# Performance work log

Hardware: AMD Instinct MI355X
Metric: run time of the kernel (lower is better)

The kernel has to match this reference:

```python
import jax, jax.numpy as jnp
import numpy as np

N = 100000   # nodes
E = 1600000  # edges (avg degree 16)
D = 32       # feature dim

def setup_inputs() -> dict:
    key = jax.random.key(0)
    k1, k2, k3, k4 = jax.random.split(key, 4)
    feat = jax.random.normal(k1, (N, D), dtype=jnp.float32)
    e_feat = jax.random.normal(k2, (E, 1), dtype=jnp.float32)
    src = jax.random.randint(k3, (E,), 0, N)
    dst = jax.random.randint(k4, (E,), 0, N)
    return {"feat": feat, "e_feat": e_feat, "src": src, "dst": dst}

def reference(feat, e_feat, src, dst):
    n = feat.shape[0]
    ones = jnp.ones(src.shape[0], dtype=feat.dtype)
    # degrees computed on the full graph (before self-loop removal), as in DGL code
    out_deg = jax.ops.segment_sum(ones, src, num_segments=n)
    in_deg = jax.ops.segment_sum(ones, dst, num_segments=n)
    src_norm = jnp.power(jnp.clip(out_deg, 1.0, None), -0.5)[:, None]  # [N,1]
    dst_norm = jnp.power(jnp.clip(in_deg, 1.0, None), -0.5)[:, None]   # [N,1]
    # remove_self_loop: mask out self-loop edges in the aggregation only
    mask = (src != dst).astype(feat.dtype)[:, None]                    # [E,1]
    # u_mul_e: gather normalized src features, multiply by edge weight
    msg = (feat * src_norm)[src] * (e_feat * mask)                     # [E,D]
    agg = jax.ops.segment_sum(msg, dst, num_segments=n)                # [N,D]
    out = feat - agg * dst_norm
    return jnp.sum(jnp.abs(out), axis=1)                               # [N]
```

## Files before the change

### kernel.cpp

```cpp
#include <hip/hip_runtime.h>

#define D 32
#define RANGE 128
#define RMAX 800
#define JC 512
#define CHUNKMAX 3200
#define CAP 2304
#define SJC 128
#define SCHUNKMAX 12800

__global__ __launch_bounds__(512) void sort_src(
        const int* __restrict__ src,
        unsigned* __restrict__ srcs, unsigned* __restrict__ metaS,
        int E, int R, int chunkS) {
    __shared__ unsigned ids[SCHUNKMAX];
    __shared__ int cs[RMAX];
    __shared__ int cur[RMAX];
    int j = blockIdx.x, t = threadIdx.x;
    int e0 = j * chunkS, e1 = min(E, e0 + chunkS), cntE = e1 - e0;
    for (int i = t; i < RMAX; i += 512) cs[i] = 0;
    __syncthreads();
    for (int e = e0 + 2 * t; e < e1; e += 1024) {
        if (e + 1 < e1) {
            int2 s2 = *(const int2*)(src + e);
            atomicAdd(&cs[s2.x >> 7], 1);
            atomicAdd(&cs[s2.y >> 7], 1);
        } else {
            atomicAdd(&cs[src[e] >> 7], 1);
        }
    }
    __syncthreads();
    {
        int i1 = t + 512;
        cur[t] = cs[t];
        if (i1 < RMAX) cur[i1] = cs[i1];
        __syncthreads();
        for (int off = 1; off < RMAX; off <<= 1) {
            int v0 = (t >= off) ? cur[t - off] : 0;
            int v1 = 0;
            if (i1 < RMAX && i1 >= off) v1 = cur[i1 - off];
            __syncthreads();
            cur[t] += v0;
            if (i1 < RMAX) cur[i1] += v1;
            __syncthreads();
        }
        cur[t] -= cs[t];
        if (i1 < RMAX) cur[i1] -= cs[i1];
        __syncthreads();
    }
    for (int e = e0 + t; e < e1; e += 512) {
        unsigned s = (unsigned)src[e];
        int pos = atomicAdd(&cur[s >> 7], 1);
        ids[pos] = s;
    }
    __syncthreads();
    size_t baseE = (size_t)j * chunkS;
    for (int i = t; i < cntE; i += 512) srcs[baseE + i] = ids[i];
    for (int i = t; i < R; i += 512)
        metaS[(size_t)j * R + i] =
            ((unsigned)(cur[i] - cs[i]) << 16) | (unsigned)cs[i];
}

__global__ __launch_bounds__(512) void sort_chunks(
        const int* __restrict__ src, const int* __restrict__ dst,
        const float* __restrict__ ef,
        uint2* __restrict__ recs, unsigned* __restrict__ metaD,
        int E, int R, int chunk) {
    __shared__ uint2 sd[CHUNKMAX];
    __shared__ int cd[RMAX];
    __shared__ int curD[RMAX];
    int j = blockIdx.x, t = threadIdx.x;
    int e0 = j * chunk, e1 = min(E, e0 + chunk), cntE = e1 - e0;
    for (int i = t; i < RMAX; i += 512) cd[i] = 0;
    __syncthreads();
    for (int e = e0 + 2 * t; e < e1; e += 1024) {
        if (e + 1 < e1) {
            int2 d2 = *(const int2*)(dst + e);
            atomicAdd(&cd[d2.x >> 7], 1);
            atomicAdd(&cd[d2.y >> 7], 1);
        } else {
            atomicAdd(&cd[dst[e] >> 7], 1);
        }
    }
    __syncthreads();
    {
        int i1 = t + 512;
        curD[t] = cd[t];
        if (i1 < RMAX) curD[i1] = cd[i1];
        __syncthreads();
        for (int off = 1; off < RMAX; off <<= 1) {
            int v0 = (t >= off) ? curD[t - off] : 0;
            int v1 = 0;
            if (i1 < RMAX && i1 >= off) v1 = curD[i1 - off];
            __syncthreads();
            curD[t] += v0;
            if (i1 < RMAX) curD[i1] += v1;
            __syncthreads();
        }
        curD[t] -= cd[t];
        if (i1 < RMAX) curD[i1] -= cd[i1];
        __syncthreads();
    }
    for (int e = e0 + t; e < e1; e += 512) {
        int s = src[e], d = dst[e];
        float w = (s == d) ? 0.0f : ef[e];
        int pos = atomicAdd(&curD[d >> 7], 1);
        sd[pos] = make_uint2((unsigned)s | ((unsigned)(d & (RANGE - 1)) << 17),
                             __float_as_uint(w));
    }
    __syncthreads();
    size_t baseE = (size_t)j * chunk;
    for (int i = t; i < cntE; i += 512) recs[baseE + i] = sd[i];
    for (int i = t; i < R; i += 512)
        metaD[(size_t)i * JC + j] =
            ((unsigned)(curD[i] - cd[i]) << 16) | (unsigned)cd[i];
}

__device__ __forceinline__ unsigned short f2bf(float x) {
    unsigned u = __float_as_uint(x);
    u += 0x7FFFu + ((u >> 16) & 1u);
    return (unsigned short)(u >> 16);
}

__global__ __launch_bounds__(512) void srcnorm_convert(
        const unsigned* __restrict__ srcs, const unsigned* __restrict__ metaS,
        const float* __restrict__ feat, unsigned short* __restrict__ featb,
        int n, int R, int chunkS) {
    __shared__ int cnt[RANGE];
    __shared__ unsigned meta[SJC];
    int r = blockIdx.x, t = threadIdx.x;
    int base = r * RANGE, lim = min(n - base, RANGE);
    if (t < RANGE) cnt[t] = 0;
    if (t < SJC) meta[t] = metaS[(size_t)t * R + r];
    __syncthreads();
    int seg = t >> 2, sub = t & 3;
    {
        unsigned m = meta[seg];
        int st = m >> 16, c = m & 0xFFFFu;
        const unsigned* p = srcs + (size_t)seg * chunkS + st;
        for (int k = sub; k < c; k += 4)
            atomicAdd(&cnt[p[k] - (unsigned)base], 1);
    }
    __syncthreads();
    int total4 = lim * 8;
    for (int i = t; i < total4; i += 512) {
        int row = i >> 3;
        float sn = rsqrtf((float)max(cnt[row], 1));
        float4 f = ((const float4*)(feat + (size_t)(base + row) * D))[i & 7];
        ushort4 u;
        u.x = f2bf(f.x * sn); u.y = f2bf(f.y * sn);
        u.z = f2bf(f.z * sn); u.w = f2bf(f.w * sn);
        ((ushort4*)(featb + (size_t)(base + row) * D))[i & 7] = u;
    }
}

__global__ __launch_bounds__(512) void gather_kernel(
        const float* __restrict__ feat, const unsigned short* __restrict__ featb,
        const uint2* __restrict__ recs, const unsigned* __restrict__ metaD,
        float* __restrict__ out, int n, int R, int chunk) {
    __shared__ uint2 raw[CAP];
    __shared__ uint2 srec[CAP];
    __shared__ int segpre[JC + 1];
    __shared__ int indeg[RANGE];
    __shared__ int pre[RANGE + 1];
    int r = blockIdx.x, t = threadIdx.x;
    int base = r * RANGE, lim = min(n - base, RANGE);
    unsigned m = metaD[(size_t)r * JC + t];
    int st = m >> 16, c = m & 0xFFFFu;
    segpre[t + 1] = c;
    if (t == 0) segpre[0] = 0;
    if (t < RANGE) indeg[t] = 0;
    __syncthreads();
    for (int off = 1; off < JC; off <<= 1) {
        int v = (t + 1 > off) ? segpre[t + 1 - off] : 0;
        __syncthreads();
        segpre[t + 1] += v;
        __syncthreads();
    }
    int total = segpre[JC];
    bool ovf = total > CAP;
    const uint2* p = recs + (size_t)t * chunk + st;
    if (!ovf) {
        int dp = segpre[t];
        for (int k = 0; k < c; k++) {
            uint2 rec = p[k];
            raw[dp + k] = rec;
            atomicAdd(&indeg[rec.x >> 17], 1);
        }
    } else {
        for (int k = 0; k < c; k++) atomicAdd(&indeg[p[k].x >> 17], 1);
    }
    __syncthreads();
    if (t < RANGE) pre[t + 1] = indeg[t];
    if (t == 0) pre[0] = 0;
    __syncthreads();
    for (int off = 1; off < RANGE; off <<= 1) {
        int v = 0;
        if (t < RANGE) { int idx = t + 1; if (idx > off) v = pre[idx - off]; }
        __syncthreads();
        if (t < RANGE) pre[t + 1] += v;
        __syncthreads();
    }
    if (t < RANGE) indeg[t] = pre[t];
    __syncthreads();
    if (!ovf) {
        for (int i = t; i < total; i += 512) {
            uint2 rec = raw[i];
            int dl = rec.x >> 17;
            int pos = atomicAdd(&indeg[dl], 1);
            srec[pos] = make_uint2(rec.x & 0x1FFFFu, rec.y);
        }
    }
    __syncthreads();
    int node = t >> 2;
    int cch = t & 3;
    if (node >= lim) return;
    int p0i = pre[node];
    int cnt = pre[node + 1] - p0i;
    float a0 = 0.f, a1 = 0.f, a2 = 0.f, a3 = 0.f, a4 = 0.f, a5 = 0.f, a6 = 0.f, a7 = 0.f;
    if (!ovf) {
        const uint2* sp = srec + p0i;
        int i = 0;
        for (; i + 4 <= cnt; i += 4) {
            uint2 q0 = sp[i], q1 = sp[i + 1], q2 = sp[i + 2], q3 = sp[i + 3];
            uint4 b0 = ((const uint4*)(featb + (size_t)q0.x * D))[cch];
            uint4 b1 = ((const uint4*)(featb + (size_t)q1.x * D))[cch];
            uint4 b2 = ((const uint4*)(featb + (size_t)q2.x * D))[cch];
            uint4 b3 = ((const uint4*)(featb + (size_t)q3.x * D))[cch];
            float w0 = __uint_as_float(q0.y), w1 = __uint_as_float(q1.y);
            float w2 = __uint_as_float(q2.y), w3 = __uint_as_float(q3.y);
            a0 += __uint_as_float(b0.x << 16) * w0 + __uint_as_float(b1.x << 16) * w1
                + __uint_as_float(b2.x << 16) * w2 + __uint_as_float(b3.x << 16) * w3;
            a1 += __uint_as_float(b0.x & 0xFFFF0000u) * w0 + __uint_as_float(b1.x & 0xFFFF0000u) * w1
                + __uint_as_float(b2.x & 0xFFFF0000u) * w2 + __uint_as_float(b3.x & 0xFFFF0000u) * w3;
            a2 += __uint_as_float(b0.y << 16) * w0 + __uint_as_float(b1.y << 16) * w1
                + __uint_as_float(b2.y << 16) * w2 + __uint_as_float(b3.y << 16) * w3;
            a3 += __uint_as_float(b0.y & 0xFFFF0000u) * w0 + __uint_as_float(b1.y & 0xFFFF0000u) * w1
                + __uint_as_float(b2.y & 0xFFFF0000u) * w2 + __uint_as_float(b3.y & 0xFFFF0000u) * w3;
            a4 += __uint_as_float(b0.z << 16) * w0 + __uint_as_float(b1.z << 16) * w1
                + __uint_as_float(b2.z << 16) * w2 + __uint_as_float(b3.z << 16) * w3;
            a5 += __uint_as_float(b0.z & 0xFFFF0000u) * w0 + __uint_as_float(b1.z & 0xFFFF0000u) * w1
                + __uint_as_float(b2.z & 0xFFFF0000u) * w2 + __uint_as_float(b3.z & 0xFFFF0000u) * w3;
            a6 += __uint_as_float(b0.w << 16) * w0 + __uint_as_float(b1.w << 16) * w1
                + __uint_as_float(b2.w << 16) * w2 + __uint_as_float(b3.w << 16) * w3;
            a7 += __uint_as_float(b0.w & 0xFFFF0000u) * w0 + __uint_as_float(b1.w & 0xFFFF0000u) * w1
                + __uint_as_float(b2.w & 0xFFFF0000u) * w2 + __uint_as_float(b3.w & 0xFFFF0000u) * w3;
        }
        for (; i < cnt; i++) {
            uint2 q = sp[i];
            uint4 b = ((const uint4*)(featb + (size_t)q.x * D))[cch];
            float w = __uint_as_float(q.y);
            a0 += __uint_as_float(b.x << 16) * w;
            a1 += __uint_as_float(b.x & 0xFFFF0000u) * w;
            a2 += __uint_as_float(b.y << 16) * w;
            a3 += __uint_as_float(b.y & 0xFFFF0000u) * w;
            a4 += __uint_as_float(b.z << 16) * w;
            a5 += __uint_as_float(b.z & 0xFFFF0000u) * w;
            a6 += __uint_as_float(b.w << 16) * w;
            a7 += __uint_as_float(b.w & 0xFFFF0000u) * w;
        }
    } else {
        for (int j = 0; j < JC; j++) {
            unsigned mm = metaD[(size_t)r * JC + j];
            const uint2* pp = recs + (size_t)j * chunk + (mm >> 16);
            int cc = mm & 0xFFFFu;
            for (int k = 0; k < cc; k++) {
                uint2 rec = pp[k];
                if ((int)(rec.x >> 17) == node) {
                    uint4 b = ((const uint4*)(featb + (size_t)(rec.x & 0x1FFFFu) * D))[cch];
                    float w = __uint_as_float(rec.y);
                    a0 += __uint_as_float(b.x << 16) * w;
                    a1 += __uint_as_float(b.x & 0xFFFF0000u) * w;
                    a2 += __uint_as_float(b.y << 16) * w;
                    a3 += __uint_as_float(b.y & 0xFFFF0000u) * w;
                    a4 += __uint_as_float(b.z << 16) * w;
                    a5 += __uint_as_float(b.z & 0xFFFF0000u) * w;
                    a6 += __uint_as_float(b.w << 16) * w;
                    a7 += __uint_as_float(b.w & 0xFFFF0000u) * w;
                }
            }
        }
    }
    float dn = rsqrtf((float)max(cnt, 1));
    const float4* fr = (const float4*)(feat + (size_t)(base + node) * D);
    float4 fA = fr[cch * 2];
    float4 fB = fr[cch * 2 + 1];
    float v = fabsf(fA.x - a0 * dn) + fabsf(fA.y - a1 * dn) +
              fabsf(fA.z - a2 * dn) + fabsf(fA.w - a3 * dn) +
              fabsf(fB.x - a4 * dn) + fabsf(fB.y - a5 * dn) +
              fabsf(fB.z - a6 * dn) + fabsf(fB.w - a7 * dn);
    v += __shfl_xor(v, 1, 4);
    v += __shfl_xor(v, 2, 4);
    if (cch == 0) out[base + node] = v;
}

extern "C" void kernel_launch(void* const* d_in, const int* in_sizes, int n_in,
                              void* d_out, int out_size, void* d_ws, size_t ws_size,
                              hipStream_t stream) {
    const float* feat   = (const float*)d_in[0];
    const float* e_feat = (const float*)d_in[1];
    const int*   src    = (const int*)d_in[2];
    const int*   dst    = (const int*)d_in[3];
    const int E = in_sizes[2];
    const int n = in_sizes[0] / D;
    float* out = (float*)d_out;

    const int R = (n + RANGE - 1) / RANGE;
    const int chunk  = (((E + JC  - 1) / JC ) + 1) & ~1;
    const int chunkS = (((E + SJC - 1) / SJC) + 1) & ~1;

    char* p = (char*)d_ws;
    uint2* recs     = (uint2*)p;    p += ((size_t)JC * chunk * 8 + 15) & ~(size_t)15;
    unsigned* metaD = (unsigned*)p; p += ((size_t)R * JC * 4 + 15) & ~(size_t)15;
    unsigned* srcs  = (unsigned*)p; p += ((size_t)SJC * chunkS * 4 + 15) & ~(size_t)15;
    unsigned* metaS = (unsigned*)p; p += ((size_t)SJC * R * 4 + 15) & ~(size_t)15;
    unsigned short* featb = (unsigned short*)p;

    sort_src<<<SJC, 512, 0, stream>>>(src, srcs, metaS, E, R, chunkS);

    sort_chunks<<<JC, 512, 0, stream>>>(src, dst, e_feat, recs, metaD, E, R, chunk);

    srcnorm_convert<<<R, 512, 0, stream>>>(srcs, metaS, feat, featb, n, R, chunkS);

    gather_kernel<<<R, 512, 0, stream>>>(feat, featb, recs, metaD, out, n, R, chunk);
}
```

Measured before the change: 145.5 us.

## Fuse src and dst bucket sorts into one launch and use wave-shuffle scans

The two bucketing kernels (source-degree sort and destination-record sort) become a single launch in which block index picks the role, so both run concurrently and one launch is saved. The source sort is split into twice as many smaller chunks (SJC 256) to fit a shared arena and balance work. All shared-memory Hillis-Steele prefix scans are replaced by a 64-lane shuffle-based scan with a per-wave partial array, which cuts barrier counts. The trade-off is that the src blocks now share occupancy with the dst blocks, and srcnorm reads more, smaller segments.

Result: faster. 139.3 us (-4.3%).

```diff
diff --git a/kernel.cpp b/kernel.cpp
--- a/kernel.cpp
+++ b/kernel.cpp
@@ -6,114 +6,113 @@
 #define JC 512
 #define CHUNKMAX 3200
 #define CAP 2304
-#define SJC 128
-#define SCHUNKMAX 12800
-
-__global__ __launch_bounds__(512) void sort_src(
-        const int* __restrict__ src,
-        unsigned* __restrict__ srcs, unsigned* __restrict__ metaS,
-        int E, int R, int chunkS) {
-    __shared__ unsigned ids[SCHUNKMAX];
-    __shared__ int cs[RMAX];
-    __shared__ int cur[RMAX];
-    int j = blockIdx.x, t = threadIdx.x;
-    int e0 = j * chunkS, e1 = min(E, e0 + chunkS), cntE = e1 - e0;
-    for (int i = t; i < RMAX; i += 512) cs[i] = 0;
-    __syncthreads();
-    for (int e = e0 + 2 * t; e < e1; e += 1024) {
-        if (e + 1 < e1) {
-            int2 s2 = *(const int2*)(src + e);
-            atomicAdd(&cs[s2.x >> 7], 1);
-            atomicAdd(&cs[s2.y >> 7], 1);
-        } else {
-            atomicAdd(&cs[src[e] >> 7], 1);
-        }
-    }
-    __syncthreads();
-    {
-        int i1 = t + 512;
-        cur[t] = cs[t];
-        if (i1 < RMAX) cur[i1] = cs[i1];
-        __syncthreads();
-        for (int off = 1; off < RMAX; off <<= 1) {
-            int v0 = (t >= off) ? cur[t - off] : 0;
-            int v1 = 0;
-            if (i1 < RMAX && i1 >= off) v1 = cur[i1 - off];
-            __syncthreads();
-            cur[t] += v0;
-            if (i1 < RMAX) cur[i1] += v1;
-            __syncthreads();
-        }
-        cur[t] -= cs[t];
-        if (i1 < RMAX) cur[i1] -= cs[i1];
-        __syncthreads();
-    }
-    for (int e = e0 + t; e < e1; e += 512) {
-        unsigned s = (unsigned)src[e];
-        int pos = atomicAdd(&cur[s >> 7], 1);
-        ids[pos] = s;
-    }
-    __syncthreads();
-    size_t baseE = (size_t)j * chunkS;
-    for (int i = t; i < cntE; i += 512) srcs[baseE + i] = ids[i];
-    for (int i = t; i < R; i += 512)
-        metaS[(size_t)j * R + i] =
-            ((unsigned)(cur[i] - cs[i]) << 16) | (unsigned)cs[i];
-}
-
-__global__ __launch_bounds__(512) void sort_chunks(
+#define SJC 256
+#define SCHUNKMAX 6400
+
+__device__ __forceinline__ int scan512(int x, int* wp, int t) {
+    int lane = t & 63, w = t >> 6;
+    #pragma unroll
+    for (int d = 1; d < 64; d <<= 1) {
+        int y = __shfl_up(x, d, 64);
+        if (lane >= d) x += y;
+    }
+    if (lane == 63) wp[w] = x;
+    __syncthreads();
+    int off = 0;
+    #pragma unroll
+    for (int i = 0; i < 7; i++) if (i < w) off += wp[i];
+    return x + off;
+}
+
+__global__ __launch_bounds__(512) void fused_sort(
         const int* __restrict__ src, const int* __restrict__ dst,
         const float* __restrict__ ef,
         uint2* __restrict__ recs, unsigned* __restrict__ metaD,
-        int E, int R, int chunk) {
-    __shared__ uint2 sd[CHUNKMAX];
-    __shared__ int cd[RMAX];
-    __shared__ int curD[RMAX];
-    int j = blockIdx.x, t = threadIdx.x;
-    int e0 = j * chunk, e1 = min(E, e0 + chunk), cntE = e1 - e0;
-    for (int i = t; i < RMAX; i += 512) cd[i] = 0;
-    __syncthreads();
-    for (int e = e0 + 2 * t; e < e1; e += 1024) {
-        if (e + 1 < e1) {
-            int2 d2 = *(const int2*)(dst + e);
-            atomicAdd(&cd[d2.x >> 7], 1);
-            atomicAdd(&cd[d2.y >> 7], 1);
-        } else {
-            atomicAdd(&cd[dst[e] >> 7], 1);
-        }
-    }
-    __syncthreads();
-    {
+        unsigned* __restrict__ srcs, unsigned* __restrict__ metaS,
+        int E, int R, int chunk, int chunkS) {
+    __shared__ __align__(16) char arena[32000];
+    __shared__ int wp[8];
+    int t = threadIdx.x;
+    int* cnt = (int*)(arena + 25600);
+    int* cur = (int*)(arena + 28800);
+
+    if (blockIdx.x < JC) {
+        int j = blockIdx.x;
+        uint2* sd = (uint2*)arena;
+        int e0 = j * chunk, e1 = min(E, e0 + chunk), cntE = e1 - e0;
+        for (int i = t; i < RMAX; i += 512) cnt[i] = 0;
+        __syncthreads();
+        for (int e = e0 + 2 * t; e < e1; e += 1024) {
+            if (e + 1 < e1) {
+                int2 d2 = *(const int2*)(dst + e);
+                atomicAdd(&cnt[d2.x >> 7], 1);
+                atomicAdd(&cnt[d2.y >> 7], 1);
+            } else {
+                atomicAdd(&cnt[dst[e] >> 7], 1);
+            }
+        }
+        __syncthreads();
+        int v0 = cnt[t];
+        int incl0 = scan512(v0, wp, t);
+        int tot0 = wp[0] + wp[1] + wp[2] + wp[3] + wp[4] + wp[5] + wp[6] + wp[7];
+        __syncthreads();
         int i1 = t + 512;
-        curD[t] = cd[t];
-        if (i1 < RMAX) curD[i1] = cd[i1];
-        __syncthreads();
-        for (int off = 1; off < RMAX; off <<= 1) {
-            int v0 = (t >= off) ? curD[t - off] : 0;
-            int v1 = 0;
-            if (i1 < RMAX && i1 >= off) v1 = curD[i1 - off];
-            __syncthreads();
-            curD[t] += v0;
-            if (i1 < RMAX) curD[i1] += v1;
-            __syncthreads();
-        }
-        curD[t] -= cd[t];
-        if (i1 < RMAX) curD[i1] -= cd[i1];
-        __syncthreads();
-    }
-    for (int e = e0 + t; e < e1; e += 512) {
-        int s = src[e], d = dst[e];
-        float w = (s == d) ? 0.0f : ef[e];
-        int pos = atomicAdd(&curD[d >> 7], 1);
-        sd[pos] = make_uint2((unsigned)s | ((unsigned)(d & (RANGE - 1)) << 17),
-                             __float_as_uint(w));
-    }
-    __syncthreads();
-    size_t baseE = (size_t)j * chunk;
-    for (int i = t; i < cntE; i += 512) recs[baseE + i] = sd[i];
-    for (int i = t; i < R; i += 512)
-        metaD[(size_t)i * JC + j] =
-            ((unsigned)(curD[i] - cd[i]) << 16) | (unsigned)cd[i];
+        int v1 = (i1 < RMAX) ? cnt[i1] : 0;
+        int incl1 = scan512(v1, wp, t);
+        cur[t] = incl0 - v0;
+        if (i1 < RMAX) cur[i1] = tot0 + incl1 - v1;
+        __syncthreads();
+        for (int e = e0 + t; e < e1; e += 512) {
+            int s = src[e], d = dst[e];
+            float w = (s == d) ? 0.0f : ef[e];
+            int pos = atomicAdd(&cur[d >> 7], 1);
+            sd[pos] = make_uint2((unsigned)s | ((unsigned)(d & (RANGE - 1)) << 17),
+                                 __float_as_uint(w));
+        }
+        __syncthreads();
+        size_t baseE = (size_t)j * chunk;
+        for (int i = t; i < cntE; i += 512) recs[baseE + i] = sd[i];
+        for (int i = t; i < R; i += 512)
+            metaD[(size_t)i * JC + j] =
+                ((unsigned)(cur[i] - cnt[i]) << 16) | (unsigned)cnt[i];
+    } else {
+        int j = blockIdx.x - JC;
+        unsigned* ids = (unsigned*)arena;
+        int e0 = j * chunkS, e1 = min(E, e0 + chunkS), cntE = e1 - e0;
+        for (int i = t; i < RMAX; i += 512) cnt[i] = 0;
+        __syncthreads();
+        for (int e = e0 + 2 * t; e < e1; e += 1024) {
+            if (e + 1 < e1) {
+                int2 s2 = *(const int2*)(src + e);
+                atomicAdd(&cnt[s2.x >> 7], 1);
+                atomicAdd(&cnt[s2.y >> 7], 1);
+            } else {
+                atomicAdd(&cnt[src[e] >> 7], 1);
+            }
+        }
+        __syncthreads();
+        int v0 = cnt[t];
+        int incl0 = scan512(v0, wp, t);
+        int tot0 = wp[0] + wp[1] + wp[2] + wp[3] + wp[4] + wp[5] + wp[6] + wp[7];
+        __syncthreads();
+        int i1 = t + 512;
+        int v1 = (i1 < RMAX) ? cnt[i1] : 0;
+        int incl1 = scan512(v1, wp, t);
+        cur[t] = incl0 - v0;
+        if (i1 < RMAX) cur[i1] = tot0 + incl1 - v1;
+        __syncthreads();
+        for (int e = e0 + t; e < e1; e += 512) {
+            unsigned s = (unsigned)src[e];
+            int pos = atomicAdd(&cur[s >> 7], 1);
+            ids[pos] = s;
+        }
+        __syncthreads();
+        size_t baseE = (size_t)j * chunkS;
+        for (int i = t; i < cntE; i += 512) srcs[baseE + i] = ids[i];
+        for (int i = t; i < R; i += 512)
+            metaS[(size_t)j * R + i] =
+                ((unsigned)(cur[i] - cnt[i]) << 16) | (unsigned)cnt[i];
+    }
 }
 
 __device__ __forceinline__ unsigned short f2bf(float x) {
@@ -133,12 +132,12 @@
     if (t < RANGE) cnt[t] = 0;
     if (t < SJC) meta[t] = metaS[(size_t)t * R + r];
     __syncthreads();
-    int seg = t >> 2, sub = t & 3;
+    int seg = t >> 1, sub = t & 1;
     {
         unsigned m = meta[seg];
         int st = m >> 16, c = m & 0xFFFFu;
         const unsigned* p = srcs + (size_t)seg * chunkS + st;
-        for (int k = sub; k < c; k += 4)
+        for (int k = sub; k < c; k += 2)
             atomicAdd(&cnt[p[k] - (unsigned)base], 1);
     }
     __syncthreads();
@@ -160,28 +159,20 @@
         float* __restrict__ out, int n, int R, int chunk) {
     __shared__ uint2 raw[CAP];
     __shared__ uint2 srec[CAP];
-    __shared__ int segpre[JC + 1];
     __shared__ int indeg[RANGE];
     __shared__ int pre[RANGE + 1];
+    __shared__ int wp[8];
     int r = blockIdx.x, t = threadIdx.x;
     int base = r * RANGE, lim = min(n - base, RANGE);
     unsigned m = metaD[(size_t)r * JC + t];
     int st = m >> 16, c = m & 0xFFFFu;
-    segpre[t + 1] = c;
-    if (t == 0) segpre[0] = 0;
     if (t < RANGE) indeg[t] = 0;
-    __syncthreads();
-    for (int off = 1; off < JC; off <<= 1) {
-        int v = (t + 1 > off) ? segpre[t + 1 - off] : 0;
-        __syncthreads();
-        segpre[t + 1] += v;
-        __syncthreads();
-    }
-    int total = segpre[JC];
+    int incl = scan512(c, wp, t);
+    int dp = incl - c;
+    int total = wp[0] + wp[1] + wp[2] + wp[3] + wp[4] + wp[5] + wp[6] + wp[7];
     bool ovf = total > CAP;
     const uint2* p = recs + (size_t)t * chunk + st;
     if (!ovf) {
-        int dp = segpre[t];
         for (int k = 0; k < c; k++) {
             uint2 rec = p[k];
             raw[dp + k] = rec;
@@ -191,16 +182,11 @@
         for (int k = 0; k < c; k++) atomicAdd(&indeg[p[k].x >> 17], 1);
     }
     __syncthreads();
-    if (t < RANGE) pre[t + 1] = indeg[t];
+    int vv = (t < RANGE) ? indeg[t] : 0;
+    int incl2 = scan512(vv, wp, t);
+    if (t < RANGE) pre[t + 1] = incl2;
     if (t == 0) pre[0] = 0;
     __syncthreads();
-    for (int off = 1; off < RANGE; off <<= 1) {
-        int v = 0;
-        if (t < RANGE) { int idx = t + 1; if (idx > off) v = pre[idx - off]; }
-        __syncthreads();
-        if (t < RANGE) pre[t + 1] += v;
-        __syncthreads();
-    }
     if (t < RANGE) indeg[t] = pre[t];
     __syncthreads();
     if (!ovf) {
@@ -316,9 +302,8 @@
     unsigned* metaS = (unsigned*)p; p += ((size_t)SJC * R * 4 + 15) & ~(size_t)15;
     unsigned short* featb = (unsigned short*)p;
 
-    sort_src<<<SJC, 512, 0, stream>>>(src, srcs, metaS, E, R, chunkS);
-
-    sort_chunks<<<JC, 512, 0, stream>>>(src, dst, e_feat, recs, metaD, E, R, chunk);
+    fused_sort<<<JC + SJC, 512, 0, stream>>>(src, dst, e_feat, recs, metaD,
+                                             srcs, metaS, E, R, chunk, chunkS);
 
     srcnorm_convert<<<R, 512, 0, stream>>>(srcs, metaS, feat, featb, n, R, chunkS);
 
```
